# Kernel optimization log

Measured on AMD Instinct MI355X. Metric: run time of the kernel, lower is better.

Reference implementation:

```python
import jax, jax.numpy as jnp
import numpy as np


def _mask_finished_scores(score, flag):
    # score: (B, K); flag: (B, 1) bool. For finished rows: column 0 -> 0, columns > 0 -> -inf
    # (standard WeNet mask_finished_scores, applied both to (B, beam) and (B, V) tensors).
    K = score.shape[-1]
    col = jnp.arange(K)[None, :]
    score = jnp.where(flag & (col == 0), 0.0, score)
    return jnp.where(flag & (col > 0), -jnp.inf, score)


def _batch_beam_search(log_post, beam_size, masks):
    # log_post: (B, S, V) log-softmax; masks: (B, S) bool (True = padded/finished)
    B, S, V = log_post.shape
    eos = V - 1
    log_prob, idx0 = jax.lax.top_k(log_post[:, 0, :], beam_size)   # (B, beam)
    end_flag = masks[:, 0][:, None]                                # (B, 1)
    log_prob = _mask_finished_scores(log_prob, end_flag)
    idx0 = jnp.where(end_flag, eos, idx0)                          # mask_finished_preds

    def step(carry, xs):
        log_prob, end_flag = carry
        lp_i, m_i = xs                                             # (B, V), (B,)
        scores = _mask_finished_scores(lp_i, end_flag)             # (B, V)
        cand = log_prob[:, :, None] + scores[:, None, :]           # (B, beam, V)
        log_prob, top_idx = jax.lax.top_k(cand.reshape(B, beam_size * V), beam_size)
        idx = jnp.where(end_flag, eos, top_idx)                    # mask_finished_preds
        return (log_prob, m_i[:, None]), idx

    (log_prob, _), idx_rest = jax.lax.scan(
        step,
        (log_prob, end_flag),
        (jnp.swapaxes(log_post[:, 1:], 0, 1), jnp.swapaxes(masks[:, 1:], 0, 1)),
    )
    indices = jnp.concatenate([idx0[None], idx_rest], axis=0)      # (S, B, beam)
    indices = jnp.moveaxis(indices, 0, -1)                         # (B, beam, S)
    return jnp.mod(indices, V), log_prob                           # torch.fmod(indices, vocab)


def setup_inputs() -> dict:
    key = jax.random.key(0)
    k1, k2, k3 = jax.random.split(key, 3)
    B, S, V, BEAM = 16, 128, 32000, 4
    logit = jax.random.normal(k1, (B, S, V), dtype=jnp.float32)
    asd_scores = jax.random.uniform(k2, (BEAM, B), dtype=jnp.float32)
    tgt_lens = jax.random.randint(k3, (B,), 0, S)
    return {"logit": logit, "asd_scores": asd_scores, "tgt_lens": tgt_lens, "beam_size": BEAM}


def reference(logit, asd_scores, tgt_lens, beam_size):
    B, S, V = logit.shape
    lens = jnp.clip(tgt_lens, 2, S)
    # make_pad_mask(tgt_lens - 1): True where position is padding
    masks = jnp.arange(S)[None, :] >= (lens - 1)[:, None]          # (B, S) bool
    log_post = jax.nn.log_softmax(logit, axis=-1)                  # (B, S, V)
    # beam search runs under no_grad in torch -> stop_gradient here
    indices, _ = _batch_beam_search(jax.lax.stop_gradient(log_post), beam_size, masks)
    # gather per-step log-probs along each beam path: (B, beam, S)
    glp = jnp.take_along_axis(log_post[:, None], indices[..., None], axis=-1).squeeze(-1)
    topk_log_prob = jnp.sum(jnp.where(masks[:, None, :], 0.0, glp), axis=-1)  # (B, beam)
    nbest_log_dist = topk_log_prob.T                               # (beam, B)
    # compute_masd_loss_ver2 with normalized_score=True
    w = jax.nn.softmax(nbest_log_dist, axis=0)                     # exp(d - logsumexp(d, 0))
    asd_norm = asd_scores - jnp.mean(asd_scores, axis=0)           # (beam, B)
    masd = jnp.sum(w * asd_norm, axis=0)                           # (B,)
    return jnp.mean(masd)                                          # reduction='mean'
```

## Files before the change

### kernel.cpp

```cpp
#include <hip/hip_runtime.h>
#include <math.h>

#define NB 16
#define NS 128
#define NV 32000
#define ROWS (NB*NS)
#define CAP 1024
#define T0  3.0f

#define WS_IX_OFF   (ROWS*4*sizeof(float))
#define WS_PART_OFF (WS_IX_OFF + ROWS*4*sizeof(unsigned short))
#define WS_TKT_OFF  (WS_PART_OFF + 16*sizeof(float))

__device__ __forceinline__ bool lexgt(float av, int ai, float bv, int bi) {
    return (av > bv) || (av == bv && ai < bi);
}

__global__ __launch_bounds__(256)
void k_rowprep(const float* __restrict__ logit,
               float* __restrict__ ws_sc,
               unsigned short* __restrict__ ws_ix,
               unsigned int* __restrict__ ticket)
{
    const int row  = blockIdx.x;
    const int tid  = threadIdx.x;
    const int lane = tid & 63;
    const int wv   = tid >> 6;
    const float4* __restrict__ x4 = (const float4*)(logit + (size_t)row * NV);

    if (row == 0 && tid == 0) *ticket = 0u;

    __shared__ float  sM[4];
    __shared__ double sE[4];
    __shared__ int    s_cnt;
    __shared__ __align__(16) char smem[16384];
    float* s_cv = (float*)smem;
    int*   s_ci = (int*)(smem + CAP*4);
    float* stv  = (float*)smem;
    int*   sti  = (int*)(smem + 8192);

    if (tid == 0) s_cnt = 0;
    __syncthreads();

    float m = -INFINITY;
    double e0 = 0.0, e1 = 0.0, e2 = 0.0, e3 = 0.0;

#define PROC(q, base)                                                                            \
    {                                                                                            \
        float mx = fmaxf(fmaxf((q).x, (q).y), fmaxf((q).z, (q).w));                              \
        m = fmaxf(m, mx);                                                                        \
        e0 += (double)__expf((q).x);                                                             \
        e1 += (double)__expf((q).y);                                                             \
        e2 += (double)__expf((q).z);                                                             \
        e3 += (double)__expf((q).w);                                                             \
        if (mx >= T0) {                                                                          \
            if ((q).x >= T0) { int p = atomicAdd(&s_cnt, 1); if (p < CAP) { s_cv[p] = (q).x; s_ci[p] = 4*(base)+0; } } \
            if ((q).y >= T0) { int p = atomicAdd(&s_cnt, 1); if (p < CAP) { s_cv[p] = (q).y; s_ci[p] = 4*(base)+1; } } \
            if ((q).z >= T0) { int p = atomicAdd(&s_cnt, 1); if (p < CAP) { s_cv[p] = (q).z; s_ci[p] = 4*(base)+2; } } \
            if ((q).w >= T0) { int p = atomicAdd(&s_cnt, 1); if (p < CAP) { s_cv[p] = (q).w; s_ci[p] = 4*(base)+3; } } \
        }                                                                                        \
    }

    float4 a0 = x4[tid], a1 = x4[tid + 256], a2 = x4[tid + 512], a3 = x4[tid + 768];
#pragma unroll 1
    for (int k = 0; k < 6; ++k) {
        const int ib = tid + (k+1)*1024;
        float4 b0 = x4[ib];
        float4 b1 = x4[ib + 256];
        float4 b2 = x4[ib + 512];
        float4 b3 = x4[ib + 768];
        const int ia = tid + k*1024;
        PROC(a0, ia);
        PROC(a1, ia + 256);
        PROC(a2, ia + 512);
        PROC(a3, ia + 768);
        a0 = b0; a1 = b1; a2 = b2; a3 = b3;
    }
    {
        const int ia = tid + 6*1024;
        PROC(a0, ia);
        PROC(a1, ia + 256);
        PROC(a2, ia + 512);
        PROC(a3, ia + 768);
    }
    for (int i = 7168 + tid; i < NV/4; i += 256) {
        float4 q = x4[i];
        PROC(q, i);
    }
#undef PROC

    float gm = m;
    gm = fmaxf(gm, __shfl_xor(gm, 1));
    gm = fmaxf(gm, __shfl_xor(gm, 2));
    gm = fmaxf(gm, __shfl_xor(gm, 4));
    float Tw = gm;
    Tw = fminf(Tw, __shfl_xor(Tw, 8));
    Tw = fminf(Tw, __shfl_xor(Tw, 16));
    Tw = fminf(Tw, __shfl_xor(Tw, 32));
    float wm = gm;
    wm = fmaxf(wm, __shfl_xor(wm, 8));
    wm = fmaxf(wm, __shfl_xor(wm, 16));
    wm = fmaxf(wm, __shfl_xor(wm, 32));
    double es = ((e0 + e1) + (e2 + e3));
    es += __shfl_xor(es, 1);
    es += __shfl_xor(es, 2);
    es += __shfl_xor(es, 4);
    es += __shfl_xor(es, 8);
    es += __shfl_xor(es, 16);
    es += __shfl_xor(es, 32);

    if (lane == 0) { sM[wv] = wm; sE[wv] = es; }
    __syncthreads();

    const float  M    = fmaxf(fmaxf(sM[0], sM[1]), fmaxf(sM[2], sM[3]));
    const double Esum = ((sE[0] + sE[1]) + (sE[2] + sE[3]));
    int cnt = s_cnt;

    bool fast = (cnt >= 8) && (cnt <= CAP);
    if (!fast) {
        __syncthreads();
        if (tid == 0) s_cnt = 0;
        __syncthreads();
        for (int i = tid; i < NV/4; i += 256) {
            float4 q = x4[i];
            float mx = fmaxf(fmaxf(q.x, q.y), fmaxf(q.z, q.w));
            if (mx >= Tw) {
                if (q.x >= Tw) { int p = atomicAdd(&s_cnt, 1); if (p < CAP) { s_cv[p] = q.x; s_ci[p] = 4*i+0; } }
                if (q.y >= Tw) { int p = atomicAdd(&s_cnt, 1); if (p < CAP) { s_cv[p] = q.y; s_ci[p] = 4*i+1; } }
                if (q.z >= Tw) { int p = atomicAdd(&s_cnt, 1); if (p < CAP) { s_cv[p] = q.z; s_ci[p] = 4*i+2; } }
                if (q.w >= Tw) { int p = atomicAdd(&s_cnt, 1); if (p < CAP) { s_cv[p] = q.w; s_ci[p] = 4*i+3; } }
            }
        }
        __syncthreads();
        cnt = s_cnt;
    }

    if (cnt <= CAP) {
        if (wv == 0) {
            float tv[8]; int ti[8];
#pragma unroll
            for (int j = 0; j < 8; ++j) { tv[j] = -INFINITY; ti[j] = 0x7fffffff; }
            for (int c = lane; c < cnt; c += 64) {
                float v = s_cv[c]; int gi = s_ci[c];
                if (lexgt(v, gi, tv[7], ti[7])) {
                    tv[7] = v; ti[7] = gi;
#pragma unroll
                    for (int p = 7; p > 0; --p) {
                        if (lexgt(tv[p], ti[p], tv[p-1], ti[p-1])) {
                            float fv = tv[p]; tv[p] = tv[p-1]; tv[p-1] = fv;
                            int   fi = ti[p]; ti[p] = ti[p-1]; ti[p-1] = fi;
                        }
                    }
                }
            }
            float bv[8]; int bi[8];
#pragma unroll
            for (int r = 0; r < 8; ++r) {
                float hv = tv[0]; int hi = ti[0];
#pragma unroll
                for (int d = 1; d <= 32; d <<= 1) {
                    float ov = __shfl_xor(hv, d); int oi = __shfl_xor(hi, d);
                    if (lexgt(ov, oi, hv, hi)) { hv = ov; hi = oi; }
                }
                bv[r] = hv; bi[r] = hi;
                if (ti[0] == hi) {
#pragma unroll
                    for (int p = 0; p < 7; ++p) { tv[p] = tv[p+1]; ti[p] = ti[p+1]; }
                    tv[7] = -INFINITY; ti[7] = 0x7fffffff;
                }
            }
            if (lane == 0) {
                float slse = (float)(log(Esum) - (double)M);
                float sc[8]; int ix[8];
#pragma unroll
                for (int j = 0; j < 8; ++j) { sc[j] = (bv[j] - M) - slse; ix[j] = bi[j]; }
#pragma unroll
                for (int pass = 0; pass < 8; ++pass) {
#pragma unroll
                    for (int j = 0; j < 7; ++j) {
                        if (lexgt(sc[j+1], ix[j+1], sc[j], ix[j])) {
                            float fv = sc[j]; sc[j] = sc[j+1]; sc[j+1] = fv;
                            int   fi = ix[j]; ix[j] = ix[j+1]; ix[j+1] = fi;
                        }
                    }
                }
#pragma unroll
                for (int j = 0; j < 4; ++j) {
                    ws_sc[row*4+j] = sc[j];
                    ws_ix[row*4+j] = (unsigned short)ix[j];
                }
            }
        }
    } else {
        float tv[8]; int ti[8];
#pragma unroll
        for (int j = 0; j < 8; ++j) { tv[j] = -INFINITY; ti[j] = 0x7fffffff; }
        for (int i = tid; i < NV/4; i += 256) {
            float4 q = x4[i];
#pragma unroll
            for (int c = 0; c < 4; ++c) {
                float v = (c==0)?q.x:(c==1)?q.y:(c==2)?q.z:q.w;
                int gi = 4*i + c;
                if (lexgt(v, gi, tv[7], ti[7])) {
                    tv[7] = v; ti[7] = gi;
#pragma unroll
                    for (int p = 7; p > 0; --p) {
                        if (lexgt(tv[p], ti[p], tv[p-1], ti[p-1])) {
                            float fv = tv[p]; tv[p] = tv[p-1]; tv[p-1] = fv;
                            int   fi = ti[p]; ti[p] = ti[p-1]; ti[p-1] = fi;
                        }
                    }
                }
            }
        }
        __syncthreads();
#pragma unroll
        for (int j = 0; j < 8; ++j) { stv[tid*8+j] = tv[j]; sti[tid*8+j] = ti[j]; }
        __syncthreads();
        for (int st = 128; st >= 1; st >>= 1) {
            if (tid < st) {
                int pa = 0, pb = 0;
                float ov[8]; int oi[8];
#pragma unroll
                for (int j = 0; j < 8; ++j) {
                    float av = stv[tid*8+pa];      int aix = sti[tid*8+pa];
                    float bv = stv[(tid+st)*8+pb]; int bix = sti[(tid+st)*8+pb];
                    bool ta = lexgt(av, aix, bv, bix);
                    ov[j] = ta ? av : bv;
                    oi[j] = ta ? aix : bix;
                    pa += ta ? 1 : 0;
                    pb += ta ? 0 : 1;
                }
#pragma unroll
                for (int j = 0; j < 8; ++j) { stv[tid*8+j] = ov[j]; sti[tid*8+j] = oi[j]; }
            }
            __syncthreads();
        }
        if (tid == 0) {
            float slse = (float)(log(Esum) - (double)M);
            float sc[8]; int ix[8];
#pragma unroll
            for (int j = 0; j < 8; ++j) { sc[j] = (stv[j] - M) - slse; ix[j] = sti[j]; }
#pragma unroll
            for (int pass = 0; pass < 8; ++pass) {
#pragma unroll
                for (int j = 0; j < 7; ++j) {
                    if (lexgt(sc[j+1], ix[j+1], sc[j], ix[j])) {
                        float fv = sc[j]; sc[j] = sc[j+1]; sc[j+1] = fv;
                        int   fi = ix[j]; ix[j] = ix[j+1]; ix[j+1] = fi;
                    }
                }
            }
#pragma unroll
            for (int j = 0; j < 4; ++j) {
                ws_sc[row*4+j] = sc[j];
                ws_ix[row*4+j] = (unsigned short)ix[j];
            }
        }
    }
}

__global__ __launch_bounds__(64)
void k_beam(const float* __restrict__ ws_sc,
            const unsigned short* __restrict__ ws_ix,
            const float* __restrict__ asd,
            const int*   __restrict__ tlen,
            float* __restrict__ ws_part,
            unsigned int* __restrict__ ticket,
            float* __restrict__ out)
{
    const int b = blockIdx.x;
    const int lane = threadIdx.x;

    __shared__ float4  Lsc[NS];
    __shared__ ushort4 Lix[NS];
    {
        const float4*  sc4p = (const float4*)ws_sc;
        const ushort4* ix4p = (const ushort4*)ws_ix;
        for (int i = lane; i < NS; i += 64) {
            Lsc[i] = sc4p[b*NS + i];
            Lix[i] = ix4p[b*NS + i];
        }
    }
    __syncthreads();

    int L = tlen[b];
    L = L < 2 ? 2 : (L > NS ? NS : L);

    const int ci = lane & 15;
    const int k  = ci >> 2;
    const int r  = ci & 3;

    float4 sc0 = Lsc[0];
    float  c   = (lane==0)?sc0.x:(lane==1)?sc0.y:(lane==2)?sc0.z:sc0.w;
    double sum = (double)c;

    float4 scN = Lsc[1]; ushort4 ixN = Lix[1];

    for (int s = 1; s <= L-2; ++s) {
        float4 sc = scN; ushort4 ix = ixN;
        scN = Lsc[s+1]; ixN = Lix[s+1];

        float myscore = (r==0)?sc.x:(r==1)?sc.y:(r==2)?sc.z:sc.w;
        int   myidx   = (r==0)?ix.x:(r==1)?ix.y:(r==2)?ix.z:ix.w;
        float mycarry = __int_as_float(__builtin_amdgcn_ds_bpermute(k << 2, __float_as_int(c)));
        float cand = mycarry + myscore;
        int   flat = k*NV + myidx;

        int g = lane >> 4;
        int rp = 0;
#pragma unroll
        for (int mm = 0; mm < 4; ++mm) {
            int j = g*4 + mm;
            float cj = __shfl(cand, j);
            int   fj = __shfl(flat, j);
            rp += ((cj > cand) || (cj == cand && fj < flat)) ? 1 : 0;
        }
        int rank = __shfl(rp, ci) + __shfl(rp, ci+16) + __shfl(rp, ci+32) + __shfl(rp, ci+48);

        int dst = (rank < 4) ? (rank << 2) : 252;
        int nc_i = __builtin_amdgcn_ds_permute(dst, __float_as_int(cand));
        int ns_i = __builtin_amdgcn_ds_permute(dst, __float_as_int(myscore));
        c = __int_as_float(nc_i);
        sum += (lane < 4) ? (double)__int_as_float(ns_i) : 0.0;
    }

    double t0 = __shfl(sum, 0), t1 = __shfl(sum, 1), t2 = __shfl(sum, 2), t3 = __shfl(sum, 3);

    if (lane == 0) {
        double mx = fmax(fmax(t0, t1), fmax(t2, t3));
        double e0 = exp(t0 - mx), e1 = exp(t1 - mx), e2 = exp(t2 - mx), e3 = exp(t3 - mx);
        double Z = e0 + e1 + e2 + e3;
        double a0 = asd[0*16 + b], a1 = asd[1*16 + b], a2 = asd[2*16 + b], a3 = asd[3*16 + b];
        double am = (a0 + a1 + a2 + a3) * 0.25;
        double masd = (e0*(a0-am) + e1*(a1-am) + e2*(a2-am) + e3*(a3-am)) / Z;
        ws_part[b] = (float)masd;
        __threadfence();
        unsigned int t = atomicAdd(ticket, 1u);
        if (t == 15u) {
            __threadfence();
            double accd = 0.0;
#pragma unroll
            for (int i = 0; i < 16; ++i) accd += (double)ws_part[i];
            out[0] = (float)(accd / 16.0);
            *ticket = 0u;
        }
    }
}

extern "C" void kernel_launch(void* const* d_in, const int* in_sizes, int n_in,
                              void* d_out, int out_size, void* d_ws, size_t ws_size,
                              hipStream_t stream) {
    const float* logit = (const float*)d_in[0];
    const float* asd   = (const float*)d_in[1];
    const int*   tlen  = (const int*)d_in[2];
    float*          ws_sc   = (float*)d_ws;
    unsigned short* ws_ix   = (unsigned short*)((char*)d_ws + WS_IX_OFF);
    float*          ws_part = (float*)((char*)d_ws + WS_PART_OFF);
    unsigned int*   ticket  = (unsigned int*)((char*)d_ws + WS_TKT_OFF);

    k_rowprep<<<ROWS, 256, 0, stream>>>(logit, ws_sc, ws_ix, ticket);
    k_beam<<<NB, 64, 0, stream>>>(ws_sc, ws_ix, asd, tlen, ws_part, ticket, (float*)d_out);
}
```

Measured before the change: 85.63 us.

## Buffer threshold candidates in registers and batch shared-memory atomics per thread

Candidates above the fixed threshold are now held in up to three registers per thread during the streaming pass and appended to shared memory with one atomicAdd per thread afterwards, instead of one shared atomic per hit inside the hot loop. A separate overflow flag sends any block where a thread saw more than three hits to the existing slow rescan path. Launch bounds now ask for 8 blocks per SM, and the rank reduction in the beam step uses xor-shuffles instead of four indexed shuffles. The per-thread register buffer adds register pressure and branches, and the occupancy hint may cause spills.

```diff
diff --git a/kernel.cpp b/kernel.cpp
--- a/kernel.cpp
+++ b/kernel.cpp
@@ -16,7 +16,7 @@
     return (av > bv) || (av == bv && ai < bi);
 }
 
-__global__ __launch_bounds__(256)
+__global__ __launch_bounds__(256, 8)
 void k_rowprep(const float* __restrict__ logit,
                float* __restrict__ ws_sc,
                unsigned short* __restrict__ ws_ix,
@@ -33,32 +33,43 @@
     __shared__ float  sM[4];
     __shared__ double sE[4];
     __shared__ int    s_cnt;
+    __shared__ int    s_ovf;
     __shared__ __align__(16) char smem[16384];
     float* s_cv = (float*)smem;
     int*   s_ci = (int*)(smem + CAP*4);
     float* stv  = (float*)smem;
     int*   sti  = (int*)(smem + 8192);
 
-    if (tid == 0) s_cnt = 0;
+    if (tid == 0) { s_cnt = 0; s_ovf = 0; }
     __syncthreads();
 
     float m = -INFINITY;
     double e0 = 0.0, e1 = 0.0, e2 = 0.0, e3 = 0.0;
-
-#define PROC(q, base)                                                                            \
-    {                                                                                            \
-        float mx = fmaxf(fmaxf((q).x, (q).y), fmaxf((q).z, (q).w));                              \
-        m = fmaxf(m, mx);                                                                        \
-        e0 += (double)__expf((q).x);                                                             \
-        e1 += (double)__expf((q).y);                                                             \
-        e2 += (double)__expf((q).z);                                                             \
-        e3 += (double)__expf((q).w);                                                             \
-        if (mx >= T0) {                                                                          \
-            if ((q).x >= T0) { int p = atomicAdd(&s_cnt, 1); if (p < CAP) { s_cv[p] = (q).x; s_ci[p] = 4*(base)+0; } } \
-            if ((q).y >= T0) { int p = atomicAdd(&s_cnt, 1); if (p < CAP) { s_cv[p] = (q).y; s_ci[p] = 4*(base)+1; } } \
-            if ((q).z >= T0) { int p = atomicAdd(&s_cnt, 1); if (p < CAP) { s_cv[p] = (q).z; s_ci[p] = 4*(base)+2; } } \
-            if ((q).w >= T0) { int p = atomicAdd(&s_cnt, 1); if (p < CAP) { s_cv[p] = (q).w; s_ci[p] = 4*(base)+3; } } \
-        }                                                                                        \
+    float rv0 = 0.f, rv1 = 0.f, rv2 = 0.f;
+    int   ri0 = 0, ri1 = 0, ri2 = 0, cnt = 0;
+
+#define INS(v, gi)                                                    \
+    {                                                                 \
+        if      (cnt == 0) { rv0 = (v); ri0 = (gi); }                 \
+        else if (cnt == 1) { rv1 = (v); ri1 = (gi); }                 \
+        else if (cnt == 2) { rv2 = (v); ri2 = (gi); }                 \
+        cnt++;                                                        \
+    }
+
+#define PROC(q, base)                                                 \
+    {                                                                 \
+        float mx = fmaxf(fmaxf((q).x, (q).y), fmaxf((q).z, (q).w));   \
+        m = fmaxf(m, mx);                                             \
+        e0 += (double)__expf((q).x);                                  \
+        e1 += (double)__expf((q).y);                                  \
+        e2 += (double)__expf((q).z);                                  \
+        e3 += (double)__expf((q).w);                                  \
+        if (mx >= T0) {                                               \
+            if ((q).x >= T0) INS((q).x, 4*(base)+0);                  \
+            if ((q).y >= T0) INS((q).y, 4*(base)+1);                  \
+            if ((q).z >= T0) INS((q).z, 4*(base)+2);                  \
+            if ((q).w >= T0) INS((q).w, 4*(base)+3);                  \
+        }                                                             \
     }
 
     float4 a0 = x4[tid], a1 = x4[tid + 256], a2 = x4[tid + 512], a3 = x4[tid + 768];
@@ -88,6 +99,7 @@
         PROC(q, i);
     }
 #undef PROC
+#undef INS
 
     float gm = m;
     gm = fmaxf(gm, __shfl_xor(gm, 1));
@@ -109,14 +121,25 @@
     es += __shfl_xor(es, 16);
     es += __shfl_xor(es, 32);
 
+    {
+        int n = cnt < 3 ? cnt : 3;
+        if (cnt > 3) atomicOr(&s_ovf, 1);
+        if (n > 0) {
+            int p = atomicAdd(&s_cnt, n);
+            s_cv[p] = rv0; s_ci[p] = ri0;
+            if (n > 1) { s_cv[p+1] = rv1; s_ci[p+1] = ri1; }
+            if (n > 2) { s_cv[p+2] = rv2; s_ci[p+2] = ri2; }
+        }
+    }
+
     if (lane == 0) { sM[wv] = wm; sE[wv] = es; }
     __syncthreads();
 
     const float  M    = fmaxf(fmaxf(sM[0], sM[1]), fmaxf(sM[2], sM[3]));
     const double Esum = ((sE[0] + sE[1]) + (sE[2] + sE[3]));
-    int cnt = s_cnt;
-
-    bool fast = (cnt >= 8) && (cnt <= CAP);
+    int cnt_blk = s_cnt;
+    const bool fast = (s_ovf == 0) && (cnt_blk >= 8);
+
     if (!fast) {
         __syncthreads();
         if (tid == 0) s_cnt = 0;
@@ -132,15 +155,15 @@
             }
         }
         __syncthreads();
-        cnt = s_cnt;
-    }
-
-    if (cnt <= CAP) {
+        cnt_blk = s_cnt;
+    }
+
+    if (cnt_blk <= CAP) {
         if (wv == 0) {
             float tv[8]; int ti[8];
 #pragma unroll
             for (int j = 0; j < 8; ++j) { tv[j] = -INFINITY; ti[j] = 0x7fffffff; }
-            for (int c = lane; c < cnt; c += 64) {
+            for (int c = lane; c < cnt_blk; c += 64) {
                 float v = s_cv[c]; int gi = s_ci[c];
                 if (lexgt(v, gi, tv[7], ti[7])) {
                     tv[7] = v; ti[7] = gi;
@@ -316,7 +339,9 @@
             int   fj = __shfl(flat, j);
             rp += ((cj > cand) || (cj == cand && fj < flat)) ? 1 : 0;
         }
-        int rank = __shfl(rp, ci) + __shfl(rp, ci+16) + __shfl(rp, ci+32) + __shfl(rp, ci+48);
+        rp += __shfl_xor(rp, 16);
+        rp += __shfl_xor(rp, 32);
+        const int rank = rp;
 
         int dst = (rank < 4) ? (rank << 2) : 252;
         int nc_i = __builtin_amdgcn_ds_permute(dst, __float_as_int(cand));
```

Result: slower. 94.71 us (+10.6%).
